# Performance work log

Hardware: AMD Instinct MI355X
Metric: run time of the kernel (lower is better)

Reference implementation:

```python
import jax, jax.numpy as jnp
import numpy as np

B, N, D, HEADS, P, C = 64, 197, 768, 12, 12, 200
ARC_S, ARC_M = 30.0, 0.5


def layer_norm(x, g, b, eps=1e-5):
    m = jnp.mean(x, axis=-1, keepdims=True)
    v = jnp.var(x, axis=-1, keepdims=True)
    return (x - m) / jnp.sqrt(v + eps) * g + b


def setup_inputs() -> dict:
    key = jax.random.key(0)
    ks = jax.random.split(key, 16)
    sc = 0.02
    return {
        'hidden': jax.random.normal(ks[0], (B, N, D), jnp.float32),
        'attns': jax.random.uniform(ks[1], (4, B, HEADS, N, N), jnp.float32),
        'labels': jax.random.randint(ks[2], (B,), 0, C),
        'ln1_g': jnp.ones((D,), jnp.float32),
        'ln1_b': jnp.zeros((D,), jnp.float32),
        'w_in': jax.random.normal(ks[3], (3 * D, D), jnp.float32) * sc,
        'b_in': jnp.zeros((3 * D,), jnp.float32),
        'w_out': jax.random.normal(ks[4], (D, D), jnp.float32) * sc,
        'b_out': jnp.zeros((D,), jnp.float32),
        'ln2_g': jnp.ones((D,), jnp.float32),
        'ln2_b': jnp.zeros((D,), jnp.float32),
        'w_pool': jax.random.normal(ks[5], (1, D), jnp.float32) * sc,
        'b_pool': jnp.zeros((1,), jnp.float32),
        'pool_temp': jnp.float32(1.0),
        'w_mlp': jax.random.normal(ks[6], (D, D), jnp.float32) * sc,
        'b_mlp': jnp.zeros((D,), jnp.float32),
        'arc_w': jax.random.normal(ks[7], (C, 2 * D), jnp.float32) * sc,
    }


def reference(hidden, attns, labels, ln1_g, ln1_b, w_in, b_in, w_out, b_out,
              ln2_g, ln2_b, w_pool, b_pool, pool_temp, w_mlp, b_mlp, arc_w):
    cls_embed = hidden[:, 0]              # [B, D]
    patch_embeds = hidden[:, 1:]          # [B, N-1, D]

    # Multi-layer attention fusion: mean over heads, CLS row, drop CLS col.
    attn_scores = attns.mean(axis=2)[:, :, 0, 1:].mean(axis=0)  # [B, N-1]

    # Top-k part selection + gather.
    idx = jax.lax.top_k(attn_scores, P)[1]                       # [B, P]
    parts = jnp.take_along_axis(patch_embeds, idx[:, :, None], axis=1)  # [B,P,D]
    parts = layer_norm(parts, ln1_g, ln1_b)

    # Multi-head self-attention over parts (eval mode, no dropout).
    hd = D // HEADS
    qkv = parts @ w_in.T + b_in                                  # [B,P,3D]
    q, k, v = jnp.split(qkv, 3, axis=-1)
    def heads(t):
        return t.reshape(B, P, HEADS, hd).transpose(0, 2, 1, 3)  # [B,H,P,hd]
    q, k, v = heads(q), heads(k), heads(v)
    scores = jnp.einsum('bhqd,bhkd->bhqk', q, k) / jnp.sqrt(jnp.float32(hd))
    a = jax.nn.softmax(scores, axis=-1)
    o = jnp.einsum('bhqk,bhkd->bhqd', a, v)
    o = o.transpose(0, 2, 1, 3).reshape(B, P, D)
    attn_out = o @ w_out.T + b_out
    attn_out = layer_norm(attn_out, ln2_g, ln2_b)

    # Temperature-softmax weighted pooling.
    raw_w = (attn_out @ w_pool.T + b_pool)[..., 0]               # [B,P]
    weights = jax.nn.softmax(raw_w / jnp.maximum(pool_temp, 0.3), axis=1)
    part_feat = jnp.sum(attn_out * weights[..., None], axis=1)   # [B,D]
    part_feat = jax.nn.relu(part_feat @ w_mlp.T + b_mlp)

    fusion = jnp.concatenate([cls_embed, part_feat], axis=1)     # [B,2D]

    # ArcFace margin (train logits with labels).
    fn = fusion / jnp.linalg.norm(fusion, axis=-1, keepdims=True)
    wn = arc_w / jnp.linalg.norm(arc_w, axis=-1, keepdims=True)
    cosine = fn @ wn.T                                           # [B,C]
    sine = jnp.sqrt(jnp.clip(1.0 - cosine ** 2, 0.0, 1.0))
    cos_m, sin_m = np.cos(ARC_M), np.sin(ARC_M)
    th = np.cos(np.pi - ARC_M)
    mm = np.sin(np.pi - ARC_M) * ARC_M
    phi = cosine * cos_m - sine * sin_m
    phi = jnp.where(cosine > th, phi, cosine - mm)
    one_hot = jax.nn.one_hot(labels, C, dtype=cosine.dtype)
    logits = (one_hot * phi + (1.0 - one_hot) * cosine) * ARC_S
    return logits
```

## Files before the change

### kernel.cpp

```cpp
#include <hip/hip_runtime.h>
#include <hip/hip_bf16.h>
#include <float.h>
#include <math.h>

#define BB 64
#define NNtok 197
#define DD 768
#define HH 12
#define PP 12
#define CC 200
#define NPATCH 196

typedef short bf16x8 __attribute__((ext_vector_type(8)));
typedef float f32x4 __attribute__((ext_vector_type(4)));

__device__ __forceinline__ unsigned short bf16_bits(float x) {
  __hip_bfloat16 h = __float2bfloat16(x);
  return *reinterpret_cast<unsigned short*>(&h);
}
__device__ __forceinline__ float u2f(unsigned int u) {
  union { unsigned int u; float f; } cv; cv.u = u; return cv.f;
}
__device__ __forceinline__ float bfu(unsigned short us) {
  union { unsigned int u; float f; } cv; cv.u = ((unsigned int)us) << 16; return cv.f;
}

__global__ __launch_bounds__(256) void k1_front(
    const float* __restrict__ hidden, const float* __restrict__ attns,
    const float* __restrict__ g, const float* __restrict__ be,
    const float* __restrict__ w1, const float* __restrict__ w2,
    const float* __restrict__ w3, __hip_bfloat16* __restrict__ o1,
    __hip_bfloat16* __restrict__ o2, __hip_bfloat16* __restrict__ o3,
    __hip_bfloat16* __restrict__ parts) {
  int t = threadIdx.x, bi = blockIdx.x;
  if (bi >= 64) {
    for (int i = (bi - 64) * 256 + t; i < 737280; i += 256 * 256) {
      const float* src; __hip_bfloat16* dst; int off;
      if (i < 442368) { src = w1; dst = o1; off = i; }
      else if (i < 589824) { src = w2; dst = o2; off = i - 442368; }
      else { src = w3; dst = o3; off = i - 589824; }
      float4 v = ((const float4*)src)[off];
      union { unsigned short u[4]; ushort4 v4; } p;
      p.u[0] = bf16_bits(v.x); p.u[1] = bf16_bits(v.y);
      p.u[2] = bf16_bits(v.z); p.u[3] = bf16_bits(v.w);
      ((ushort4*)dst)[off] = p.v4;
    }
    return;
  }
  int b = bi;
  __shared__ float sc[256];
  __shared__ int sel_s[PP];
  int wv = t >> 6, ln = t & 63;
  float acc = -FLT_MAX;
  if (t < NPATCH) {
    acc = 0.f;
#pragma unroll
    for (int l = 0; l < 4; l++) {
      float part = 0.f;
#pragma unroll
      for (int h = 0; h < HH; h++) {
        size_t base = (size_t)((l * BB + b) * HH + h) * ((size_t)NNtok * NNtok);
        part += attns[base + 1 + t];
      }
      acc += part * (1.f / 12.f);
    }
    acc *= 0.25f;
  }
  sc[t] = acc;
  __syncthreads();
  if (t < 64) {
    float v[4]; int idx[4];
#pragma unroll
    for (int j = 0; j < 4; j++) { idx[j] = t + j * 64; v[j] = sc[idx[j]]; }
    for (int it = 0; it < PP; ++it) {
      float bv = v[0]; int bidx = idx[0];
#pragma unroll
      for (int j = 1; j < 4; j++)
        if (v[j] > bv || (v[j] == bv && idx[j] < bidx)) { bv = v[j]; bidx = idx[j]; }
      float cv = bv; int ci = bidx;
#pragma unroll
      for (int off = 32; off > 0; off >>= 1) {
        float ov = __shfl_xor(cv, off); int oi = __shfl_xor(ci, off);
        if (ov > cv || (ov == cv && oi < ci)) { cv = ov; ci = oi; }
      }
      if (t == 0) sel_s[it] = ci;
#pragma unroll
      for (int j = 0; j < 4; j++)
        if (idx[j] == ci) v[j] = -FLT_MAX;
    }
  }
  __syncthreads();
#pragma unroll
  for (int q = 0; q < 3; q++) {
    int i = wv * 3 + q;
    const float* row = hidden + ((size_t)b * NNtok + 1 + sel_s[i]) * DD;
    float x[12], s1 = 0.f, s2 = 0.f;
#pragma unroll
    for (int k = 0; k < 12; k++) {
      x[k] = row[ln + 64 * k];
      s1 += x[k]; s2 += x[k] * x[k];
    }
#pragma unroll
    for (int off = 32; off > 0; off >>= 1) {
      s1 += __shfl_xor(s1, off); s2 += __shfl_xor(s2, off);
    }
    float m = s1 * (1.f / DD);
    float rstd = rsqrtf(s2 * (1.f / DD) - m * m + 1e-5f);
    __hip_bfloat16* outp_ = parts + ((size_t)b * PP + i) * DD;
#pragma unroll
    for (int k = 0; k < 12; k++) {
      int d = ln + 64 * k;
      outp_[d] = __float2bfloat16((x[k] - m) * rstd * g[d] + be[d]);
    }
  }
}

__global__ __launch_bounds__(256) void k2_mid(
    const __hip_bfloat16* __restrict__ parts, const __hip_bfloat16* __restrict__ w_in_bf,
    const float* __restrict__ b_in, const __hip_bfloat16* __restrict__ w_out_bf,
    float* __restrict__ part_ws) {
  int bi = blockIdx.x;
  int b = bi >> 2, hg = bi & 3;
  int t = threadIdx.x;
  int wave = t >> 6, lane = t & 63, lr = lane & 15, kg = lane >> 4;
  __shared__ __align__(16) unsigned short qkv3[3][16][192];
  __shared__ __align__(16) unsigned short o3[16][192];
  __shared__ float scores[432];

  int pr = lr < 12 ? lr : 11;
  const __hip_bfloat16* Ab = parts + ((size_t)b * 12 + pr) * DD + kg * 8;
  int wrow[9];
#pragma unroll
  for (int nf = 0; nf < 9; nf++) {
    int lc = wave * 144 + nf * 16 + lr;
    int s = lc / 192, d2 = lc - s * 192;
    wrow[nf] = s * 768 + hg * 192 + d2;
  }
  f32x4 acc[9];
#pragma unroll
  for (int nf = 0; nf < 9; nf++) { acc[nf][0]=0.f; acc[nf][1]=0.f; acc[nf][2]=0.f; acc[nf][3]=0.f; }
  for (int k0 = 0; k0 < 768; k0 += 32) {
    bf16x8 af = *(const bf16x8*)(Ab + k0);
    bf16x8 wf[9];
#pragma unroll
    for (int nf = 0; nf < 9; nf++)
      wf[nf] = *(const bf16x8*)(w_in_bf + (size_t)wrow[nf] * DD + kg * 8 + k0);
#pragma unroll
    for (int nf = 0; nf < 9; nf++)
      acc[nf] = __builtin_amdgcn_mfma_f32_16x16x32_bf16(af, wf[nf], acc[nf], 0, 0, 0);
  }
#pragma unroll
  for (int nf = 0; nf < 9; nf++) {
    int lc = wave * 144 + nf * 16 + lr;
    int s = lc / 192, d2 = lc - s * 192;
    float bv = b_in[s * 768 + hg * 192 + d2];
#pragma unroll
    for (int r = 0; r < 4; r++) {
      int p = kg * 4 + r;
      qkv3[s][p][d2] = bf16_bits(acc[nf][r] + bv);
    }
  }
  __syncthreads();

  for (int e = t; e < 432; e += 256) {
    int h = e / 144, rem = e - h * 144;
    int i = rem / 12, j = rem - i * 12;
    float s = 0.f;
#pragma unroll
    for (int d = 0; d < 64; d++)
      s += bfu(qkv3[0][i][h * 64 + d]) * bfu(qkv3[1][j][h * 64 + d]);
    scores[e] = s * 0.125f;
  }
  __syncthreads();
  if (t < 36) {
    int h = t / 12, i = t - h * 12;
    float* row = scores + h * 144 + i * 12;
    float m = -FLT_MAX;
#pragma unroll
    for (int j = 0; j < 12; j++) m = fmaxf(m, row[j]);
    float e2[12], sum = 0.f;
#pragma unroll
    for (int j = 0; j < 12; j++) { e2[j] = expf(row[j] - m); sum += e2[j]; }
    float inv = 1.f / sum;
#pragma unroll
    for (int j = 0; j < 12; j++) row[j] = e2[j] * inv;
  }
  __syncthreads();
  for (int o = t; o < 2304; o += 256) {
    int i = o / 192, d2 = o - i * 192;
    int h = d2 >> 6;
    float s = 0.f;
#pragma unroll
    for (int j = 0; j < 12; j++)
      s += scores[h * 144 + i * 12 + j] * bfu(qkv3[2][j][d2]);
    o3[i][d2] = bf16_bits(s);
  }
  __syncthreads();

  f32x4 acc2[12];
#pragma unroll
  for (int jf = 0; jf < 12; jf++) { acc2[jf][0]=0.f; acc2[jf][1]=0.f; acc2[jf][2]=0.f; acc2[jf][3]=0.f; }
  const unsigned short* Ob = &o3[0][0] + lr * 192 + kg * 8;
  for (int k0 = 0; k0 < 192; k0 += 32) {
    bf16x8 af = *(const bf16x8*)(Ob + k0);
    bf16x8 wf[12];
#pragma unroll
    for (int jf = 0; jf < 12; jf++) {
      int j = wave * 192 + jf * 16 + lr;
      wf[jf] = *(const bf16x8*)(w_out_bf + (size_t)j * DD + hg * 192 + kg * 8 + k0);
    }
#pragma unroll
    for (int jf = 0; jf < 12; jf++)
      acc2[jf] = __builtin_amdgcn_mfma_f32_16x16x32_bf16(af, wf[jf], acc2[jf], 0, 0, 0);
  }
#pragma unroll
  for (int jf = 0; jf < 12; jf++) {
    int j = wave * 192 + jf * 16 + lr;
#pragma unroll
    for (int r = 0; r < 4; r++) {
      int p = kg * 4 + r;
      if (p < 12)
        part_ws[(((size_t)b * 4 + hg) * 12 + p) * DD + j] = acc2[jf][r];
    }
  }
}

__global__ __launch_bounds__(256) void k3_back(
    const float* __restrict__ part_ws, const float* __restrict__ b_out,
    const float* __restrict__ g, const float* __restrict__ be,
    const float* __restrict__ wp, const float* __restrict__ bp,
    const float* __restrict__ ptemp, const __hip_bfloat16* __restrict__ wmlp,
    const float* __restrict__ bmlp, float* __restrict__ pmlp) {
  int bi = blockIdx.x;
  int b = bi >> 2, q4 = bi & 3;
  int t = threadIdx.x, wv = t >> 6, ln = t & 63;
  __shared__ float a12[12 * 768];
  __shared__ float raww_s[12];
  __shared__ float pfeat[768];
  for (int u = t; u < 9216; u += 256) {
    int j = u % 768;
    float s = b_out[j];
#pragma unroll
    for (int hg = 0; hg < 4; hg++)
      s += part_ws[(((size_t)b * 4 + hg) * 12) * DD + u];
    a12[u] = s;
  }
  __syncthreads();
#pragma unroll
  for (int q = 0; q < 3; q++) {
    int r = wv * 3 + q;
    float x[12], s1 = 0.f, s2 = 0.f;
#pragma unroll
    for (int k = 0; k < 12; k++) {
      x[k] = a12[r * 768 + ln + 64 * k];
      s1 += x[k]; s2 += x[k] * x[k];
    }
#pragma unroll
    for (int off = 32; off > 0; off >>= 1) {
      s1 += __shfl_xor(s1, off); s2 += __shfl_xor(s2, off);
    }
    float m = s1 * (1.f / DD);
    float rstd = rsqrtf(s2 * (1.f / DD) - m * m + 1e-5f);
    float pl = 0.f;
#pragma unroll
    for (int k = 0; k < 12; k++) {
      int d = ln + 64 * k;
      float y = (x[k] - m) * rstd * g[d] + be[d];
      a12[r * 768 + d] = y;
      pl += y * wp[d];
    }
#pragma unroll
    for (int off = 32; off > 0; off >>= 1) pl += __shfl_xor(pl, off);
    if (ln == 0) raww_s[r] = pl + bp[0];
  }
  __syncthreads();
  float wts[12];
  {
    float inv = 1.f / fmaxf(ptemp[0], 0.3f);
    float z[12], mx = -FLT_MAX;
#pragma unroll
    for (int p = 0; p < 12; p++) { z[p] = raww_s[p] * inv; mx = fmaxf(mx, z[p]); }
    float s = 0.f;
#pragma unroll
    for (int p = 0; p < 12; p++) { z[p] = expf(z[p] - mx); s += z[p]; }
    float is = 1.f / s;
#pragma unroll
    for (int p = 0; p < 12; p++) wts[p] = z[p] * is;
  }
  for (int d = t; d < 768; d += 256) {
    float s = 0.f;
#pragma unroll
    for (int p = 0; p < 12; p++) s += a12[p * 768 + d] * wts[p];
    pfeat[d] = s;
  }
  __syncthreads();
  if (t < 192) {
    int j = q4 * 192 + t;
    const uint4* wr = (const uint4*)(wmlp + (size_t)j * DD);
    float acc2 = bmlp[j];
    for (int k = 0; k < 96; k++) {
      uint4 w4 = wr[k];
      const float* pf = &pfeat[k * 8];
      acc2 += pf[0] * u2f(w4.x << 16) + pf[1] * u2f(w4.x & 0xFFFF0000u)
            + pf[2] * u2f(w4.y << 16) + pf[3] * u2f(w4.y & 0xFFFF0000u)
            + pf[4] * u2f(w4.z << 16) + pf[5] * u2f(w4.z & 0xFFFF0000u)
            + pf[6] * u2f(w4.w << 16) + pf[7] * u2f(w4.w & 0xFFFF0000u);
    }
    pmlp[(size_t)b * DD + j] = fmaxf(acc2, 0.f);
  }
}

__global__ __launch_bounds__(256) void k4_arc(
    const float* __restrict__ hidden, const float* __restrict__ pmlp,
    const float* __restrict__ aw, const int* __restrict__ labels,
    float* __restrict__ out) {
  int cb = blockIdx.x, b = blockIdx.y, t = threadIdx.x;
  int wv = t >> 6, ln = t & 63;
  __shared__ float4 fs4[384];
  __shared__ float a4[4];
  const float4* cls4 = (const float4*)(hidden + (size_t)b * NNtok * DD);
  const float4* pm4 = (const float4*)(pmlp + (size_t)b * DD);
  for (int u = t; u < 384; u += 256) fs4[u] = (u < 192) ? cls4[u] : pm4[u - 192];
  __syncthreads();
  float s = 0.f;
  for (int u = t; u < 384; u += 256) {
    float4 v = fs4[u];
    s += v.x * v.x + v.y * v.y + v.z * v.z + v.w * v.w;
  }
#pragma unroll
  for (int off = 32; off > 0; off >>= 1) s += __shfl_xor(s, off);
  if (ln == 0) a4[wv] = s;
  __syncthreads();
  float rnf = rsqrtf(a4[0] + a4[1] + a4[2] + a4[3]);
  int lab = labels[b];
  const float cos_m = 0.8775825618903728f, sin_m = 0.479425538604203f;
  const float th = -0.8775825618903728f, mm = 0.2397127693021015f;
#pragma unroll
  for (int ci = 0; ci < 4; ci++) {
    int c = cb * 16 + ci * 4 + wv;
    if (c < CC) {
      const float4* wr = (const float4*)(aw + (size_t)c * 1536);
      float acc = 0.f, nw = 0.f;
#pragma unroll
      for (int k = 0; k < 6; k++) {
        float4 a = fs4[ln + 64 * k];
        float4 w = wr[ln + 64 * k];
        acc += a.x * w.x + a.y * w.y + a.z * w.z + a.w * w.w;
        nw += w.x * w.x + w.y * w.y + w.z * w.z + w.w * w.w;
      }
#pragma unroll
      for (int off = 32; off > 0; off >>= 1) {
        acc += __shfl_xor(acc, off); nw += __shfl_xor(nw, off);
      }
      if (ln == 0) {
        float cosv = acc * rsqrtf(nw) * rnf;
        float s2 = 1.f - cosv * cosv;
        s2 = fminf(fmaxf(s2, 0.f), 1.f);
        float sinv = sqrtf(s2);
        float phi = cosv * cos_m - sinv * sin_m;
        phi = (cosv > th) ? phi : (cosv - mm);
        out[(size_t)b * CC + c] = ((c == lab) ? phi : cosv) * 30.f;
      }
    }
  }
}

extern "C" void kernel_launch(void* const* d_in, const int* in_sizes, int n_in,
                              void* d_out, int out_size, void* d_ws, size_t ws_size,
                              hipStream_t stream) {
  const float* hidden = (const float*)d_in[0];
  const float* attns  = (const float*)d_in[1];
  const int*   labels = (const int*)d_in[2];
  const float* ln1_g  = (const float*)d_in[3];
  const float* ln1_b  = (const float*)d_in[4];
  const float* w_in   = (const float*)d_in[5];
  const float* b_in   = (const float*)d_in[6];
  const float* w_out  = (const float*)d_in[7];
  const float* b_out  = (const float*)d_in[8];
  const float* ln2_g  = (const float*)d_in[9];
  const float* ln2_b  = (const float*)d_in[10];
  const float* w_pool = (const float*)d_in[11];
  const float* b_pool = (const float*)d_in[12];
  const float* ptemp  = (const float*)d_in[13];
  const float* w_mlp  = (const float*)d_in[14];
  const float* b_mlp  = (const float*)d_in[15];
  const float* arc_w  = (const float*)d_in[16];
  float* outp = (float*)d_out;

  float* F = (float*)d_ws;
  float* part_ws = F;
  float* pmlp    = F + 2359296;
  __hip_bfloat16* parts_bf = (__hip_bfloat16*)(F + 2408448);
  __hip_bfloat16* w_in_bf  = (__hip_bfloat16*)(F + 2703360);
  __hip_bfloat16* w_out_bf = (__hip_bfloat16*)(F + 3588096);
  __hip_bfloat16* w_mlp_bf = (__hip_bfloat16*)(F + 3883008);

  k1_front<<<320, 256, 0, stream>>>(hidden, attns, ln1_g, ln1_b, w_in, w_out,
                                    w_mlp, w_in_bf, w_out_bf, w_mlp_bf, parts_bf);
  k2_mid<<<256, 256, 0, stream>>>(parts_bf, w_in_bf, b_in, w_out_bf, part_ws);
  k3_back<<<256, 256, 0, stream>>>(part_ws, b_out, ln2_g, ln2_b, w_pool, b_pool,
                                   ptemp, w_mlp_bf, b_mlp, pmlp);
  k4_arc<<<dim3(13, BB), 256, 0, stream>>>(hidden, pmlp, arc_w, labels, outp);
}
```

Measured before the change: 90.79 us.

## Fuse front, attention, pooling and ArcFace into one per-sample kernel

Replaces the four-kernel pipeline with a weight-cast kernel plus one 1024-thread block per batch sample that does top-k selection, LayerNorm, QKV projection, attention, output projection, pooling, MLP and ArcFace entirely in shared memory with XOR-swizzled layouts. This removes the global round trips for parts, per-head-group partial outputs and pooled features, plus two launches. The cost is only 64 blocks on a large GPU, so each block streams the full weight matrices and all of arc_w, giving low parallelism and heavy per-block weight traffic.

After: 205.9 us. +126.7%, slower.

```diff
diff --git a/kernel.cpp b/kernel.cpp
--- a/kernel.cpp
+++ b/kernel.cpp
@@ -10,8 +10,10 @@
 #define PP 12
 #define CC 200
 #define NPATCH 196
+#define QSTR 2312
 
 typedef short bf16x8 __attribute__((ext_vector_type(8)));
+typedef short bf16x4 __attribute__((ext_vector_type(4)));
 typedef float f32x4 __attribute__((ext_vector_type(4)));
 
 __device__ __forceinline__ unsigned short bf16_bits(float x) {
@@ -25,234 +27,242 @@
   union { unsigned int u; float f; } cv; cv.u = ((unsigned int)us) << 16; return cv.f;
 }
 
-__global__ __launch_bounds__(256) void k1_front(
-    const float* __restrict__ hidden, const float* __restrict__ attns,
-    const float* __restrict__ g, const float* __restrict__ be,
+__global__ __launch_bounds__(256) void k1_cast(
     const float* __restrict__ w1, const float* __restrict__ w2,
     const float* __restrict__ w3, __hip_bfloat16* __restrict__ o1,
-    __hip_bfloat16* __restrict__ o2, __hip_bfloat16* __restrict__ o3,
-    __hip_bfloat16* __restrict__ parts) {
-  int t = threadIdx.x, bi = blockIdx.x;
-  if (bi >= 64) {
-    for (int i = (bi - 64) * 256 + t; i < 737280; i += 256 * 256) {
-      const float* src; __hip_bfloat16* dst; int off;
-      if (i < 442368) { src = w1; dst = o1; off = i; }
-      else if (i < 589824) { src = w2; dst = o2; off = i - 442368; }
-      else { src = w3; dst = o3; off = i - 589824; }
-      float4 v = ((const float4*)src)[off];
-      union { unsigned short u[4]; ushort4 v4; } p;
-      p.u[0] = bf16_bits(v.x); p.u[1] = bf16_bits(v.y);
-      p.u[2] = bf16_bits(v.z); p.u[3] = bf16_bits(v.w);
-      ((ushort4*)dst)[off] = p.v4;
-    }
-    return;
-  }
-  int b = bi;
-  __shared__ float sc[256];
-  __shared__ int sel_s[PP];
+    __hip_bfloat16* __restrict__ o2, __hip_bfloat16* __restrict__ o3) {
+  for (int i = blockIdx.x * 256 + threadIdx.x; i < 737280; i += 256 * 256) {
+    const float* src; __hip_bfloat16* dst; int off;
+    if (i < 442368) { src = w1; dst = o1; off = i; }
+    else if (i < 589824) { src = w2; dst = o2; off = i - 442368; }
+    else { src = w3; dst = o3; off = i - 589824; }
+    float4 v = ((const float4*)src)[off];
+    union { unsigned short u[4]; ushort4 v4; } p;
+    p.u[0] = bf16_bits(v.x); p.u[1] = bf16_bits(v.y);
+    p.u[2] = bf16_bits(v.z); p.u[3] = bf16_bits(v.w);
+    ((ushort4*)dst)[off] = p.v4;
+  }
+}
+
+__global__ __launch_bounds__(1024, 4) void k2_all(
+    const float* __restrict__ hidden, const float* __restrict__ attns,
+    const int* __restrict__ labels, const float* __restrict__ ln1_g,
+    const float* __restrict__ ln1_b, const __hip_bfloat16* __restrict__ w_in_bf,
+    const float* __restrict__ b_in, const __hip_bfloat16* __restrict__ w_out_bf,
+    const float* __restrict__ b_out, const float* __restrict__ ln2_g,
+    const float* __restrict__ ln2_b, const float* __restrict__ w_pool,
+    const float* __restrict__ b_pool, const float* __restrict__ ptemp,
+    const __hip_bfloat16* __restrict__ w_mlp_bf, const float* __restrict__ b_mlp,
+    const float* __restrict__ arc_w, float* __restrict__ out) {
+  __shared__ __align__(16) char sm[80832];
+  int t = threadIdx.x, b = blockIdx.x;
   int wv = t >> 6, ln = t & 63;
-  float acc = -FLT_MAX;
-  if (t < NPATCH) {
-    acc = 0.f;
-#pragma unroll
-    for (int l = 0; l < 4; l++) {
+  char* A = sm;
+  char* Bz = sm + 18432;
+  float* scoresC = (float*)(sm + 73920);
+
+  {
+    float* sgrp = (float*)Bz;
+    float* sc = (float*)(Bz + 4096);
+    int* sel = (int*)(Bz + 5120);
+    int g = t >> 8, p = t & 255;
+    if (p < NPATCH) {
       float part = 0.f;
 #pragma unroll
       for (int h = 0; h < HH; h++) {
-        size_t base = (size_t)((l * BB + b) * HH + h) * ((size_t)NNtok * NNtok);
-        part += attns[base + 1 + t];
-      }
-      acc += part * (1.f / 12.f);
-    }
-    acc *= 0.25f;
-  }
-  sc[t] = acc;
-  __syncthreads();
-  if (t < 64) {
-    float v[4]; int idx[4];
-#pragma unroll
-    for (int j = 0; j < 4; j++) { idx[j] = t + j * 64; v[j] = sc[idx[j]]; }
-    for (int it = 0; it < PP; ++it) {
-      float bv = v[0]; int bidx = idx[0];
-#pragma unroll
-      for (int j = 1; j < 4; j++)
-        if (v[j] > bv || (v[j] == bv && idx[j] < bidx)) { bv = v[j]; bidx = idx[j]; }
-      float cv = bv; int ci = bidx;
+        size_t base = (size_t)((g * BB + b) * HH + h) * ((size_t)NNtok * NNtok);
+        part += attns[base + 1 + p];
+      }
+      sgrp[g * 256 + p] = part;
+    }
+    __syncthreads();
+    if (t < 256) {
+      float acc = -FLT_MAX;
+      if (t < NPATCH)
+        acc = (sgrp[t] * (1.f / 12.f) + sgrp[256 + t] * (1.f / 12.f) +
+               sgrp[512 + t] * (1.f / 12.f) + sgrp[768 + t] * (1.f / 12.f)) * 0.25f;
+      sc[t] = acc;
+    }
+    __syncthreads();
+    if (t < 64) {
+      float v[4]; int idx[4];
+#pragma unroll
+      for (int j = 0; j < 4; j++) { idx[j] = t + j * 64; v[j] = sc[idx[j]]; }
+      for (int it = 0; it < PP; ++it) {
+        float bv = v[0]; int bidx = idx[0];
+#pragma unroll
+        for (int j = 1; j < 4; j++)
+          if (v[j] > bv || (v[j] == bv && idx[j] < bidx)) { bv = v[j]; bidx = idx[j]; }
+        float cv = bv; int ci = bidx;
+#pragma unroll
+        for (int off = 32; off > 0; off >>= 1) {
+          float ov = __shfl_xor(cv, off); int oi = __shfl_xor(ci, off);
+          if (ov > cv || (ov == cv && oi < ci)) { cv = ov; ci = oi; }
+        }
+        if (t == 0) sel[it] = ci;
+#pragma unroll
+        for (int j = 0; j < 4; j++)
+          if (idx[j] == ci) v[j] = -FLT_MAX;
+      }
+    }
+    __syncthreads();
+    if (wv < 12) {
+      int i = wv;
+      const float* row = hidden + ((size_t)b * NNtok + 1 + sel[i]) * DD;
+      float x[12], s1 = 0.f, s2 = 0.f;
+#pragma unroll
+      for (int k = 0; k < 12; k++) {
+        x[k] = row[ln + 64 * k];
+        s1 += x[k]; s2 += x[k] * x[k];
+      }
 #pragma unroll
       for (int off = 32; off > 0; off >>= 1) {
-        float ov = __shfl_xor(cv, off); int oi = __shfl_xor(ci, off);
-        if (ov > cv || (ov == cv && oi < ci)) { cv = ov; ci = oi; }
-      }
-      if (t == 0) sel_s[it] = ci;
-#pragma unroll
-      for (int j = 0; j < 4; j++)
-        if (idx[j] == ci) v[j] = -FLT_MAX;
-    }
-  }
-  __syncthreads();
-#pragma unroll
-  for (int q = 0; q < 3; q++) {
-    int i = wv * 3 + q;
-    const float* row = hidden + ((size_t)b * NNtok + 1 + sel_s[i]) * DD;
+        s1 += __shfl_xor(s1, off); s2 += __shfl_xor(s2, off);
+      }
+      float m = s1 * (1.f / DD);
+      float rstd = rsqrtf(s2 * (1.f / DD) - m * m + 1e-5f);
+      int sw = (i & 7) << 4;
+#pragma unroll
+      for (int k = 0; k < 12; k++) {
+        int d = ln + 64 * k;
+        *(unsigned short*)(A + i * 1536 + ((2 * d) ^ sw)) =
+            bf16_bits((x[k] - m) * rstd * ln1_g[d] + ln1_b[d]);
+      }
+    }
+  }
+  __syncthreads();
+
+  {
+    int lr = ln & 15, kg = ln >> 4;
+    int pr = lr < 12 ? lr : 11;
+    int asw = (pr & 7) << 4;
+    f32x4 acc[9];
+#pragma unroll
+    for (int nf = 0; nf < 9; nf++) { acc[nf][0]=0.f; acc[nf][1]=0.f; acc[nf][2]=0.f; acc[nf][3]=0.f; }
+    for (int m = 0; m < 24; m++) {
+      bf16x8 af = *(const bf16x8*)(A + pr * 1536 + ((kg * 16 + m * 64) ^ asw));
+      bf16x8 wf[9];
+#pragma unroll
+      for (int nf = 0; nf < 9; nf++) {
+        int j = wv * 144 + nf * 16 + lr;
+        wf[nf] = *(const bf16x8*)(w_in_bf + (size_t)j * DD + kg * 8 + m * 32);
+      }
+#pragma unroll
+      for (int nf = 0; nf < 9; nf++)
+        acc[nf] = __builtin_amdgcn_mfma_f32_16x16x32_bf16(af, wf[nf], acc[nf], 0, 0, 0);
+    }
+    unsigned short* qkv = (unsigned short*)Bz;
+#pragma unroll
+    for (int nf = 0; nf < 9; nf++) {
+      int j = wv * 144 + nf * 16 + lr;
+      float bv = b_in[j];
+#pragma unroll
+      for (int r = 0; r < 4; r++) {
+        int p = kg * 4 + r;
+        if (p < 12) qkv[p * QSTR + j] = bf16_bits(acc[nf][r] + bv);
+      }
+    }
+  }
+  __syncthreads();
+
+  {
+    const unsigned short* qkv = (const unsigned short*)Bz;
+    for (int e = t; e < 1728; e += 1024) {
+      int h = e / 144, rem = e - h * 144, i = rem / 12, j = rem - i * 12;
+      const unsigned short* qp = qkv + i * QSTR + h * 64;
+      const unsigned short* kp = qkv + j * QSTR + 768 + h * 64;
+      float s = 0.f;
+#pragma unroll
+      for (int d4 = 0; d4 < 16; d4++) {
+        bf16x4 q4 = *(const bf16x4*)(qp + d4 * 4);
+        bf16x4 k4 = *(const bf16x4*)(kp + d4 * 4);
+#pragma unroll
+        for (int e2 = 0; e2 < 4; e2++)
+          s += bfu((unsigned short)q4[e2]) * bfu((unsigned short)k4[e2]);
+      }
+      scoresC[e] = s * 0.125f;
+    }
+    __syncthreads();
+    if (t < 144) {
+      int h = t / 12, i = t - h * 12;
+      float* row = scoresC + h * 144 + i * 12;
+      float m = -FLT_MAX;
+#pragma unroll
+      for (int j = 0; j < 12; j++) m = fmaxf(m, row[j]);
+      float e2[12], sum = 0.f;
+#pragma unroll
+      for (int j = 0; j < 12; j++) { e2[j] = expf(row[j] - m); sum += e2[j]; }
+      float inv = 1.f / sum;
+#pragma unroll
+      for (int j = 0; j < 12; j++) row[j] = e2[j] * inv;
+    }
+    __syncthreads();
+    for (int q = t; q < 2304; q += 1024) {
+      int i = q / 192, c4 = (q - i * 192) * 4;
+      int h = c4 >> 6;
+      const float* prow = scoresC + h * 144 + i * 12;
+      float o0 = 0.f, o1 = 0.f, o2 = 0.f, o3v = 0.f;
+#pragma unroll
+      for (int j = 0; j < 12; j++) {
+        bf16x4 v4 = *(const bf16x4*)(qkv + j * QSTR + 1536 + c4);
+        float p = prow[j];
+        o0 += p * bfu((unsigned short)v4[0]);
+        o1 += p * bfu((unsigned short)v4[1]);
+        o2 += p * bfu((unsigned short)v4[2]);
+        o3v += p * bfu((unsigned short)v4[3]);
+      }
+      bf16x4 ov;
+      ov[0] = (short)bf16_bits(o0); ov[1] = (short)bf16_bits(o1);
+      ov[2] = (short)bf16_bits(o2); ov[3] = (short)bf16_bits(o3v);
+      *(bf16x4*)(A + i * 1536 + ((2 * c4) ^ ((i & 7) << 4))) = ov;
+    }
+  }
+  __syncthreads();
+
+  {
+    int lr = ln & 15, kg = ln >> 4;
+    int pr = lr < 12 ? lr : 11;
+    int asw = (pr & 7) << 4;
+    f32x4 acc[3];
+#pragma unroll
+    for (int jf = 0; jf < 3; jf++) { acc[jf][0]=0.f; acc[jf][1]=0.f; acc[jf][2]=0.f; acc[jf][3]=0.f; }
+    for (int m = 0; m < 24; m++) {
+      bf16x8 af = *(const bf16x8*)(A + pr * 1536 + ((kg * 16 + m * 64) ^ asw));
+      bf16x8 wf[3];
+#pragma unroll
+      for (int jf = 0; jf < 3; jf++) {
+        int j = wv * 48 + jf * 16 + lr;
+        wf[jf] = *(const bf16x8*)(w_out_bf + (size_t)j * DD + kg * 8 + m * 32);
+      }
+#pragma unroll
+      for (int jf = 0; jf < 3; jf++)
+        acc[jf] = __builtin_amdgcn_mfma_f32_16x16x32_bf16(af, wf[jf], acc[jf], 0, 0, 0);
+    }
+    float* aout = (float*)Bz;
+#pragma unroll
+    for (int jf = 0; jf < 3; jf++) {
+      int j = wv * 48 + jf * 16 + lr;
+      float bv = b_out[j];
+#pragma unroll
+      for (int r = 0; r < 4; r++) {
+        int p = kg * 4 + r;
+        if (p < 12) aout[p * DD + j] = acc[jf][r] + bv;
+      }
+    }
+  }
+  __syncthreads();
+
+  float* aout = (float*)Bz;
+  float* pfeat = (float*)(Bz + 36864);
+  float* fs = (float*)(Bz + 39936);
+  float* raww = (float*)(Bz + 46080);
+  float* a16 = (float*)(Bz + 46128);
+  if (wv < 12) {
+    int r = wv;
     float x[12], s1 = 0.f, s2 = 0.f;
 #pragma unroll
     for (int k = 0; k < 12; k++) {
-      x[k] = row[ln + 64 * k];
-      s1 += x[k]; s2 += x[k] * x[k];
-    }
-#pragma unroll
-    for (int off = 32; off > 0; off >>= 1) {
-      s1 += __shfl_xor(s1, off); s2 += __shfl_xor(s2, off);
-    }
-    float m = s1 * (1.f / DD);
-    float rstd = rsqrtf(s2 * (1.f / DD) - m * m + 1e-5f);
-    __hip_bfloat16* outp_ = parts + ((size_t)b * PP + i) * DD;
-#pragma unroll
-    for (int k = 0; k < 12; k++) {
-      int d = ln + 64 * k;
-      outp_[d] = __float2bfloat16((x[k] - m) * rstd * g[d] + be[d]);
-    }
-  }
-}
-
-__global__ __launch_bounds__(256) void k2_mid(
-    const __hip_bfloat16* __restrict__ parts, const __hip_bfloat16* __restrict__ w_in_bf,
-    const float* __restrict__ b_in, const __hip_bfloat16* __restrict__ w_out_bf,
-    float* __restrict__ part_ws) {
-  int bi = blockIdx.x;
-  int b = bi >> 2, hg = bi & 3;
-  int t = threadIdx.x;
-  int wave = t >> 6, lane = t & 63, lr = lane & 15, kg = lane >> 4;
-  __shared__ __align__(16) unsigned short qkv3[3][16][192];
-  __shared__ __align__(16) unsigned short o3[16][192];
-  __shared__ float scores[432];
-
-  int pr = lr < 12 ? lr : 11;
-  const __hip_bfloat16* Ab = parts + ((size_t)b * 12 + pr) * DD + kg * 8;
-  int wrow[9];
-#pragma unroll
-  for (int nf = 0; nf < 9; nf++) {
-    int lc = wave * 144 + nf * 16 + lr;
-    int s = lc / 192, d2 = lc - s * 192;
-    wrow[nf] = s * 768 + hg * 192 + d2;
-  }
-  f32x4 acc[9];
-#pragma unroll
-  for (int nf = 0; nf < 9; nf++) { acc[nf][0]=0.f; acc[nf][1]=0.f; acc[nf][2]=0.f; acc[nf][3]=0.f; }
-  for (int k0 = 0; k0 < 768; k0 += 32) {
-    bf16x8 af = *(const bf16x8*)(Ab + k0);
-    bf16x8 wf[9];
-#pragma unroll
-    for (int nf = 0; nf < 9; nf++)
-      wf[nf] = *(const bf16x8*)(w_in_bf + (size_t)wrow[nf] * DD + kg * 8 + k0);
-#pragma unroll
-    for (int nf = 0; nf < 9; nf++)
-      acc[nf] = __builtin_amdgcn_mfma_f32_16x16x32_bf16(af, wf[nf], acc[nf], 0, 0, 0);
-  }
-#pragma unroll
-  for (int nf = 0; nf < 9; nf++) {
-    int lc = wave * 144 + nf * 16 + lr;
-    int s = lc / 192, d2 = lc - s * 192;
-    float bv = b_in[s * 768 + hg * 192 + d2];
-#pragma unroll
-    for (int r = 0; r < 4; r++) {
-      int p = kg * 4 + r;
-      qkv3[s][p][d2] = bf16_bits(acc[nf][r] + bv);
-    }
-  }
-  __syncthreads();
-
-  for (int e = t; e < 432; e += 256) {
-    int h = e / 144, rem = e - h * 144;
-    int i = rem / 12, j = rem - i * 12;
-    float s = 0.f;
-#pragma unroll
-    for (int d = 0; d < 64; d++)
-      s += bfu(qkv3[0][i][h * 64 + d]) * bfu(qkv3[1][j][h * 64 + d]);
-    scores[e] = s * 0.125f;
-  }
-  __syncthreads();
-  if (t < 36) {
-    int h = t / 12, i = t - h * 12;
-    float* row = scores + h * 144 + i * 12;
-    float m = -FLT_MAX;
-#pragma unroll
-    for (int j = 0; j < 12; j++) m = fmaxf(m, row[j]);
-    float e2[12], sum = 0.f;
-#pragma unroll
-    for (int j = 0; j < 12; j++) { e2[j] = expf(row[j] - m); sum += e2[j]; }
-    float inv = 1.f / sum;
-#pragma unroll
-    for (int j = 0; j < 12; j++) row[j] = e2[j] * inv;
-  }
-  __syncthreads();
-  for (int o = t; o < 2304; o += 256) {
-    int i = o / 192, d2 = o - i * 192;
-    int h = d2 >> 6;
-    float s = 0.f;
-#pragma unroll
-    for (int j = 0; j < 12; j++)
-      s += scores[h * 144 + i * 12 + j] * bfu(qkv3[2][j][d2]);
-    o3[i][d2] = bf16_bits(s);
-  }
-  __syncthreads();
-
-  f32x4 acc2[12];
-#pragma unroll
-  for (int jf = 0; jf < 12; jf++) { acc2[jf][0]=0.f; acc2[jf][1]=0.f; acc2[jf][2]=0.f; acc2[jf][3]=0.f; }
-  const unsigned short* Ob = &o3[0][0] + lr * 192 + kg * 8;
-  for (int k0 = 0; k0 < 192; k0 += 32) {
-    bf16x8 af = *(const bf16x8*)(Ob + k0);
-    bf16x8 wf[12];
-#pragma unroll
-    for (int jf = 0; jf < 12; jf++) {
-      int j = wave * 192 + jf * 16 + lr;
-      wf[jf] = *(const bf16x8*)(w_out_bf + (size_t)j * DD + hg * 192 + kg * 8 + k0);
-    }
-#pragma unroll
-    for (int jf = 0; jf < 12; jf++)
-      acc2[jf] = __builtin_amdgcn_mfma_f32_16x16x32_bf16(af, wf[jf], acc2[jf], 0, 0, 0);
-  }
-#pragma unroll
-  for (int jf = 0; jf < 12; jf++) {
-    int j = wave * 192 + jf * 16 + lr;
-#pragma unroll
-    for (int r = 0; r < 4; r++) {
-      int p = kg * 4 + r;
-      if (p < 12)
-        part_ws[(((size_t)b * 4 + hg) * 12 + p) * DD + j] = acc2[jf][r];
-    }
-  }
-}
-
-__global__ __launch_bounds__(256) void k3_back(
-    const float* __restrict__ part_ws, const float* __restrict__ b_out,
-    const float* __restrict__ g, const float* __restrict__ be,
-    const float* __restrict__ wp, const float* __restrict__ bp,
-    const float* __restrict__ ptemp, const __hip_bfloat16* __restrict__ wmlp,
-    const float* __restrict__ bmlp, float* __restrict__ pmlp) {
-  int bi = blockIdx.x;
-  int b = bi >> 2, q4 = bi & 3;
-  int t = threadIdx.x, wv = t >> 6, ln = t & 63;
-  __shared__ float a12[12 * 768];
-  __shared__ float raww_s[12];
-  __shared__ float pfeat[768];
-  for (int u = t; u < 9216; u += 256) {
-    int j = u % 768;
-    float s = b_out[j];
-#pragma unroll
-    for (int hg = 0; hg < 4; hg++)
-      s += part_ws[(((size_t)b * 4 + hg) * 12) * DD + u];
-    a12[u] = s;
-  }
-  __syncthreads();
-#pragma unroll
-  for (int q = 0; q < 3; q++) {
-    int r = wv * 3 + q;
-    float x[12], s1 = 0.f, s2 = 0.f;
-#pragma unroll
-    for (int k = 0; k < 12; k++) {
-      x[k] = a12[r * 768 + ln + 64 * k];
+      x[k] = aout[r * DD + ln + 64 * k];
       s1 += x[k]; s2 += x[k] * x[k];
     }
 #pragma unroll
@@ -265,39 +275,40 @@
 #pragma unroll
     for (int k = 0; k < 12; k++) {
       int d = ln + 64 * k;
-      float y = (x[k] - m) * rstd * g[d] + be[d];
-      a12[r * 768 + d] = y;
-      pl += y * wp[d];
+      float y = (x[k] - m) * rstd * ln2_g[d] + ln2_b[d];
+      aout[r * DD + d] = y;
+      pl += y * w_pool[d];
     }
 #pragma unroll
     for (int off = 32; off > 0; off >>= 1) pl += __shfl_xor(pl, off);
-    if (ln == 0) raww_s[r] = pl + bp[0];
-  }
-  __syncthreads();
-  float wts[12];
-  {
+    if (ln == 0) raww[r] = pl + b_pool[0];
+  }
+  __syncthreads();
+  {
+    float wts[12];
     float inv = 1.f / fmaxf(ptemp[0], 0.3f);
     float z[12], mx = -FLT_MAX;
 #pragma unroll
-    for (int p = 0; p < 12; p++) { z[p] = raww_s[p] * inv; mx = fmaxf(mx, z[p]); }
-    float s = 0.f;
-#pragma unroll
-    for (int p = 0; p < 12; p++) { z[p] = expf(z[p] - mx); s += z[p]; }
-    float is = 1.f / s;
+    for (int p = 0; p < 12; p++) { z[p] = raww[p] * inv; mx = fmaxf(mx, z[p]); }
+    float sme = 0.f;
+#pragma unroll
+    for (int p = 0; p < 12; p++) { z[p] = expf(z[p] - mx); sme += z[p]; }
+    float is = 1.f / sme;
 #pragma unroll
     for (int p = 0; p < 12; p++) wts[p] = z[p] * is;
-  }
-  for (int d = t; d < 768; d += 256) {
-    float s = 0.f;
-#pragma unroll
-    for (int p = 0; p < 12; p++) s += a12[p * 768 + d] * wts[p];
-    pfeat[d] = s;
-  }
-  __syncthreads();
-  if (t < 192) {
-    int j = q4 * 192 + t;
-    const uint4* wr = (const uint4*)(wmlp + (size_t)j * DD);
-    float acc2 = bmlp[j];
+    if (t < 768) {
+      float s = 0.f;
+#pragma unroll
+      for (int p = 0; p < 12; p++) s += aout[p * DD + t] * wts[p];
+      pfeat[t] = s;
+      fs[t] = hidden[(size_t)b * NNtok * DD + t];
+    }
+  }
+  __syncthreads();
+
+  if (t < 768) {
+    const uint4* wr = (const uint4*)(w_mlp_bf + (size_t)t * DD);
+    float acc2 = b_mlp[t];
     for (int k = 0; k < 96; k++) {
       uint4 w4 = wr[k];
       const float* pf = &pfeat[k * 8];
@@ -306,47 +317,38 @@
             + pf[4] * u2f(w4.z << 16) + pf[5] * u2f(w4.z & 0xFFFF0000u)
             + pf[6] * u2f(w4.w << 16) + pf[7] * u2f(w4.w & 0xFFFF0000u);
     }
-    pmlp[(size_t)b * DD + j] = fmaxf(acc2, 0.f);
-  }
-}
-
-__global__ __launch_bounds__(256) void k4_arc(
-    const float* __restrict__ hidden, const float* __restrict__ pmlp,
-    const float* __restrict__ aw, const int* __restrict__ labels,
-    float* __restrict__ out) {
-  int cb = blockIdx.x, b = blockIdx.y, t = threadIdx.x;
-  int wv = t >> 6, ln = t & 63;
-  __shared__ float4 fs4[384];
-  __shared__ float a4[4];
-  const float4* cls4 = (const float4*)(hidden + (size_t)b * NNtok * DD);
-  const float4* pm4 = (const float4*)(pmlp + (size_t)b * DD);
-  for (int u = t; u < 384; u += 256) fs4[u] = (u < 192) ? cls4[u] : pm4[u - 192];
-  __syncthreads();
-  float s = 0.f;
-  for (int u = t; u < 384; u += 256) {
-    float4 v = fs4[u];
-    s += v.x * v.x + v.y * v.y + v.z * v.z + v.w * v.w;
-  }
-#pragma unroll
-  for (int off = 32; off > 0; off >>= 1) s += __shfl_xor(s, off);
-  if (ln == 0) a4[wv] = s;
-  __syncthreads();
-  float rnf = rsqrtf(a4[0] + a4[1] + a4[2] + a4[3]);
-  int lab = labels[b];
-  const float cos_m = 0.8775825618903728f, sin_m = 0.479425538604203f;
-  const float th = -0.8775825618903728f, mm = 0.2397127693021015f;
-#pragma unroll
-  for (int ci = 0; ci < 4; ci++) {
-    int c = cb * 16 + ci * 4 + wv;
-    if (c < CC) {
-      const float4* wr = (const float4*)(aw + (size_t)c * 1536);
+    fs[768 + t] = fmaxf(acc2, 0.f);
+  }
+  __syncthreads();
+
+  {
+    float s = fs[t] * fs[t];
+    if (t < 512) { float v = fs[t + 1024]; s += v * v; }
+#pragma unroll
+    for (int off = 32; off > 0; off >>= 1) s += __shfl_xor(s, off);
+    if (ln == 0) a16[wv] = s;
+  }
+  __syncthreads();
+  float rnf;
+  {
+    float tot = 0.f;
+#pragma unroll
+    for (int i = 0; i < 16; i++) tot += a16[i];
+    rnf = rsqrtf(tot);
+  }
+
+  {
+    int lab = labels[b];
+    const float cos_m = 0.8775825618903728f, sin_m = 0.479425538604203f;
+    const float th = -0.8775825618903728f, mm = 0.2397127693021015f;
+    for (int c = wv; c < CC; c += 16) {
+      const float* wr = arc_w + (size_t)c * 1536;
       float acc = 0.f, nw = 0.f;
 #pragma unroll
-      for (int k = 0; k < 6; k++) {
-        float4 a = fs4[ln + 64 * k];
-        float4 w = wr[ln + 64 * k];
-        acc += a.x * w.x + a.y * w.y + a.z * w.z + a.w * w.w;
-        nw += w.x * w.x + w.y * w.y + w.z * w.z + w.w * w.w;
+      for (int k = 0; k < 24; k++) {
+        int d = ln + 64 * k;
+        float a = fs[d], w = wr[d];
+        acc += a * w; nw += w * w;
       }
 #pragma unroll
       for (int off = 32; off > 0; off >>= 1) {
@@ -388,17 +390,13 @@
   float* outp = (float*)d_out;
 
   float* F = (float*)d_ws;
-  float* part_ws = F;
-  float* pmlp    = F + 2359296;
-  __hip_bfloat16* parts_bf = (__hip_bfloat16*)(F + 2408448);
-  __hip_bfloat16* w_in_bf  = (__hip_bfloat16*)(F + 2703360);
-  __hip_bfloat16* w_out_bf = (__hip_bfloat16*)(F + 3588096);
-  __hip_bfloat16* w_mlp_bf = (__hip_bfloat16*)(F + 3883008);
-
-  k1_front<<<320, 256, 0, stream>>>(hidden, attns, ln1_g, ln1_b, w_in, w_out,
-                                    w_mlp, w_in_bf, w_out_bf, w_mlp_bf, parts_bf);
-  k2_mid<<<256, 256, 0, stream>>>(parts_bf, w_in_bf, b_in, w_out_bf, part_ws);
-  k3_back<<<256, 256, 0, stream>>>(part_ws, b_out, ln2_g, ln2_b, w_pool, b_pool,
-                                   ptemp, w_mlp_bf, b_mlp, pmlp);
-  k4_arc<<<dim3(13, BB), 256, 0, stream>>>(hidden, pmlp, arc_w, labels, outp);
-}
+  __hip_bfloat16* w_in_bf  = (__hip_bfloat16*)F;
+  __hip_bfloat16* w_out_bf = (__hip_bfloat16*)(F + 884736);
+  __hip_bfloat16* w_mlp_bf = (__hip_bfloat16*)(F + 1179648);
+
+  k1_cast<<<256, 256, 0, stream>>>(w_in, w_out, w_mlp, w_in_bf, w_out_bf,
+                                   w_mlp_bf);
+  k2_all<<<BB, 1024, 0, stream>>>(hidden, attns, labels, ln1_g, ln1_b, w_in_bf,
+                                  b_in, w_out_bf, b_out, ln2_g, ln2_b, w_pool,
+                                  b_pool, ptemp, w_mlp_bf, b_mlp, arc_w, outp);
+}
```

## Fuse pooling/MLP tail and ArcFace kernels into one per-batch kernel

Applied to the files above, without the earlier changes.

Merges the post-attention LayerNorm, softmax pooling and MLP kernel with the ArcFace logits kernel into a single kernel, one block per batch row. The pmlp workspace round trip and one launch go away. In exchange the grid drops from 256 plus 832 blocks to 64 blocks, each doing the full 768-wide MLP and all 200 class dot products with scalar rather than float4 loads, so parallelism falls sharply.

After: 143.9 us. 58.5% more time.

```diff
diff --git a/kernel.cpp b/kernel.cpp
--- a/kernel.cpp
+++ b/kernel.cpp
@@ -225,25 +225,28 @@
   }
 }
 
-__global__ __launch_bounds__(256) void k3_back(
+__global__ __launch_bounds__(256) void k3_tail(
     const float* __restrict__ part_ws, const float* __restrict__ b_out,
     const float* __restrict__ g, const float* __restrict__ be,
     const float* __restrict__ wp, const float* __restrict__ bp,
     const float* __restrict__ ptemp, const __hip_bfloat16* __restrict__ wmlp,
-    const float* __restrict__ bmlp, float* __restrict__ pmlp) {
-  int bi = blockIdx.x;
-  int b = bi >> 2, q4 = bi & 3;
+    const float* __restrict__ bmlp, const float* __restrict__ hidden,
+    const float* __restrict__ arc_w, const int* __restrict__ labels,
+    float* __restrict__ out) {
+  int b = blockIdx.x;
   int t = threadIdx.x, wv = t >> 6, ln = t & 63;
-  __shared__ float a12[12 * 768];
-  __shared__ float raww_s[12];
+  __shared__ __align__(16) float aout[12 * 768];
   __shared__ float pfeat[768];
+  __shared__ __align__(16) float fs[1536];
+  __shared__ float raww[12];
+  __shared__ float a4[4];
   for (int u = t; u < 9216; u += 256) {
     int j = u % 768;
     float s = b_out[j];
 #pragma unroll
-    for (int hg = 0; hg < 4; hg++)
-      s += part_ws[(((size_t)b * 4 + hg) * 12) * DD + u];
-    a12[u] = s;
+    for (int g4 = 0; g4 < 4; g4++)
+      s += part_ws[(((size_t)b * 4 + g4) * 12) * DD + u];
+    aout[u] = s;
   }
   __syncthreads();
 #pragma unroll
@@ -252,7 +255,7 @@
     float x[12], s1 = 0.f, s2 = 0.f;
 #pragma unroll
     for (int k = 0; k < 12; k++) {
-      x[k] = a12[r * 768 + ln + 64 * k];
+      x[k] = aout[r * DD + ln + 64 * k];
       s1 += x[k]; s2 += x[k] * x[k];
     }
 #pragma unroll
@@ -266,36 +269,36 @@
     for (int k = 0; k < 12; k++) {
       int d = ln + 64 * k;
       float y = (x[k] - m) * rstd * g[d] + be[d];
-      a12[r * 768 + d] = y;
+      aout[r * DD + d] = y;
       pl += y * wp[d];
     }
 #pragma unroll
     for (int off = 32; off > 0; off >>= 1) pl += __shfl_xor(pl, off);
-    if (ln == 0) raww_s[r] = pl + bp[0];
-  }
-  __syncthreads();
-  float wts[12];
+    if (ln == 0) raww[r] = pl + bp[0];
+  }
+  __syncthreads();
   {
+    float wts[12];
     float inv = 1.f / fmaxf(ptemp[0], 0.3f);
     float z[12], mx = -FLT_MAX;
 #pragma unroll
-    for (int p = 0; p < 12; p++) { z[p] = raww_s[p] * inv; mx = fmaxf(mx, z[p]); }
-    float s = 0.f;
-#pragma unroll
-    for (int p = 0; p < 12; p++) { z[p] = expf(z[p] - mx); s += z[p]; }
-    float is = 1.f / s;
+    for (int p = 0; p < 12; p++) { z[p] = raww[p] * inv; mx = fmaxf(mx, z[p]); }
+    float sme = 0.f;
+#pragma unroll
+    for (int p = 0; p < 12; p++) { z[p] = expf(z[p] - mx); sme += z[p]; }
+    float is = 1.f / sme;
 #pragma unroll
     for (int p = 0; p < 12; p++) wts[p] = z[p] * is;
-  }
-  for (int d = t; d < 768; d += 256) {
-    float s = 0.f;
-#pragma unroll
-    for (int p = 0; p < 12; p++) s += a12[p * 768 + d] * wts[p];
-    pfeat[d] = s;
-  }
-  __syncthreads();
-  if (t < 192) {
-    int j = q4 * 192 + t;
+    for (int d = t; d < 768; d += 256) {
+      float s = 0.f;
+#pragma unroll
+      for (int p = 0; p < 12; p++) s += aout[p * DD + d] * wts[p];
+      pfeat[d] = s;
+      fs[d] = hidden[(size_t)b * NNtok * DD + d];
+    }
+  }
+  __syncthreads();
+  for (int j = t; j < 768; j += 256) {
     const uint4* wr = (const uint4*)(wmlp + (size_t)j * DD);
     float acc2 = bmlp[j];
     for (int k = 0; k < 96; k++) {
@@ -306,47 +309,30 @@
             + pf[4] * u2f(w4.z << 16) + pf[5] * u2f(w4.z & 0xFFFF0000u)
             + pf[6] * u2f(w4.w << 16) + pf[7] * u2f(w4.w & 0xFFFF0000u);
     }
-    pmlp[(size_t)b * DD + j] = fmaxf(acc2, 0.f);
-  }
-}
-
-__global__ __launch_bounds__(256) void k4_arc(
-    const float* __restrict__ hidden, const float* __restrict__ pmlp,
-    const float* __restrict__ aw, const int* __restrict__ labels,
-    float* __restrict__ out) {
-  int cb = blockIdx.x, b = blockIdx.y, t = threadIdx.x;
-  int wv = t >> 6, ln = t & 63;
-  __shared__ float4 fs4[384];
-  __shared__ float a4[4];
-  const float4* cls4 = (const float4*)(hidden + (size_t)b * NNtok * DD);
-  const float4* pm4 = (const float4*)(pmlp + (size_t)b * DD);
-  for (int u = t; u < 384; u += 256) fs4[u] = (u < 192) ? cls4[u] : pm4[u - 192];
-  __syncthreads();
-  float s = 0.f;
-  for (int u = t; u < 384; u += 256) {
-    float4 v = fs4[u];
-    s += v.x * v.x + v.y * v.y + v.z * v.z + v.w * v.w;
-  }
-#pragma unroll
-  for (int off = 32; off > 0; off >>= 1) s += __shfl_xor(s, off);
-  if (ln == 0) a4[wv] = s;
+    fs[768 + j] = fmaxf(acc2, 0.f);
+  }
+  __syncthreads();
+  {
+    float s = 0.f;
+    for (int u = t; u < 1536; u += 256) { float v = fs[u]; s += v * v; }
+#pragma unroll
+    for (int off = 32; off > 0; off >>= 1) s += __shfl_xor(s, off);
+    if (ln == 0) a4[wv] = s;
+  }
   __syncthreads();
   float rnf = rsqrtf(a4[0] + a4[1] + a4[2] + a4[3]);
-  int lab = labels[b];
-  const float cos_m = 0.8775825618903728f, sin_m = 0.479425538604203f;
-  const float th = -0.8775825618903728f, mm = 0.2397127693021015f;
-#pragma unroll
-  for (int ci = 0; ci < 4; ci++) {
-    int c = cb * 16 + ci * 4 + wv;
-    if (c < CC) {
-      const float4* wr = (const float4*)(aw + (size_t)c * 1536);
+  {
+    int lab = labels[b];
+    const float cos_m = 0.8775825618903728f, sin_m = 0.479425538604203f;
+    const float th = -0.8775825618903728f, mm = 0.2397127693021015f;
+    for (int c = wv; c < CC; c += 4) {
+      const float* wr = arc_w + (size_t)c * 1536;
       float acc = 0.f, nw = 0.f;
 #pragma unroll
-      for (int k = 0; k < 6; k++) {
-        float4 a = fs4[ln + 64 * k];
-        float4 w = wr[ln + 64 * k];
-        acc += a.x * w.x + a.y * w.y + a.z * w.z + a.w * w.w;
-        nw += w.x * w.x + w.y * w.y + w.z * w.z + w.w * w.w;
+      for (int k = 0; k < 24; k++) {
+        int d = ln + 64 * k;
+        float a = fs[d], w = wr[d];
+        acc += a * w; nw += w * w;
       }
 #pragma unroll
       for (int off = 32; off > 0; off >>= 1) {
@@ -389,16 +375,15 @@
 
   float* F = (float*)d_ws;
   float* part_ws = F;
-  float* pmlp    = F + 2359296;
-  __hip_bfloat16* parts_bf = (__hip_bfloat16*)(F + 2408448);
-  __hip_bfloat16* w_in_bf  = (__hip_bfloat16*)(F + 2703360);
-  __hip_bfloat16* w_out_bf = (__hip_bfloat16*)(F + 3588096);
-  __hip_bfloat16* w_mlp_bf = (__hip_bfloat16*)(F + 3883008);
+  __hip_bfloat16* parts_bf = (__hip_bfloat16*)(F + 2359296);
+  __hip_bfloat16* w_in_bf  = (__hip_bfloat16*)(F + 2654208);
+  __hip_bfloat16* w_out_bf = (__hip_bfloat16*)(F + 3538944);
+  __hip_bfloat16* w_mlp_bf = (__hip_bfloat16*)(F + 3833856);
 
   k1_front<<<320, 256, 0, stream>>>(hidden, attns, ln1_g, ln1_b, w_in, w_out,
                                     w_mlp, w_in_bf, w_out_bf, w_mlp_bf, parts_bf);
   k2_mid<<<256, 256, 0, stream>>>(parts_bf, w_in_bf, b_in, w_out_bf, part_ws);
-  k3_back<<<256, 256, 0, stream>>>(part_ws, b_out, ln2_g, ln2_b, w_pool, b_pool,
-                                   ptemp, w_mlp_bf, b_mlp, pmlp);
-  k4_arc<<<dim3(13, BB), 256, 0, stream>>>(hidden, pmlp, arc_w, labels, outp);
-}
+  k3_tail<<<BB, 256, 0, stream>>>(part_ws, b_out, ln2_g, ln2_b, w_pool, b_pool,
+                                  ptemp, w_mlp_bf, b_mlp, hidden, arc_w, labels,
+                                  outp);
+}
```
